# Performance work log

Measured on AMD Instinct MI355X. Metric: run time of the kernel, lower is better.

The kernel has to match this reference:

```python
import jax, jax.numpy as jnp
import numpy as np

B, L, D = 256, 256, 128          # batch, max_len, embedding_dim
H = W = 16                       # H=int(sqrt(L)), W=L//H
N, CBD = 128, 1024               # embedding_num, code_book_dim = N*8 = D*8
BETA = 0.25
BN_EPS = 1e-3                    # tf.layers.batch_normalization default


def _conv(x, w, b):
    return jax.lax.conv_general_dilated(x, w, (1, 1), 'VALID',
        dimension_numbers=('NHWC', 'HWIO', 'NHWC')) + b


def _convT(x, w, b):
    return jax.lax.conv_transpose(x, w, (1, 1), 'VALID',
        dimension_numbers=('NHWC', 'HWIO', 'NHWC')) + b


def _bn(x, g, b):
    # inference-mode BN with moving_mean=0, moving_var=1 (tf.layers default training=False)
    return g * (x * (1.0 / np.sqrt(1.0 + BN_EPS))) + b


def setup_inputs() -> dict:
    key = jax.random.key(0)
    ks = jax.random.split(key, 24)
    rn = lambda k, s, sc=0.05: (jax.random.normal(k, s, dtype=jnp.float32) * sc)
    inp = {
        'x': jax.random.normal(ks[0], (B, L, D), dtype=jnp.float32),
        'mask': jnp.ones((B, L), dtype=jnp.float32),
        'code_book': jax.random.normal(ks[1], (N, CBD), dtype=jnp.float32),
        # encoder: conv2d k=2 valid, channels D -> 2D -> 4D -> 8D
        'ew1': rn(ks[2], (2, 2, D, 2 * D)), 'eb1': jnp.zeros((2 * D,), jnp.float32),
        'eg1': jnp.ones((2 * D,), jnp.float32), 'ebt1': jnp.zeros((2 * D,), jnp.float32),
        'ew2': rn(ks[3], (2, 2, 2 * D, 4 * D)), 'eb2': jnp.zeros((4 * D,), jnp.float32),
        'eg2': jnp.ones((4 * D,), jnp.float32), 'ebt2': jnp.zeros((4 * D,), jnp.float32),
        'ew3': rn(ks[4], (2, 2, 4 * D, 8 * D)), 'eb3': jnp.zeros((8 * D,), jnp.float32),
        # decoder: conv2d_transpose k=2 valid, channels 8D -> 4D -> 2D -> D
        'dw1': rn(ks[5], (2, 2, 8 * D, 4 * D)), 'db1': jnp.zeros((4 * D,), jnp.float32),
        'dg1': jnp.ones((4 * D,), jnp.float32), 'dbt1': jnp.zeros((4 * D,), jnp.float32),
        'dw2': rn(ks[6], (2, 2, 4 * D, 2 * D)), 'db2': jnp.zeros((2 * D,), jnp.float32),
        'dg2': jnp.ones((2 * D,), jnp.float32), 'dbt2': jnp.zeros((2 * D,), jnp.float32),
        'dw3': rn(ks[7], (2, 2, 2 * D, D)), 'db3': jnp.zeros((D,), jnp.float32),
    }
    return inp


def reference(x, mask, code_book,
              ew1, eb1, eg1, ebt1, ew2, eb2, eg2, ebt2, ew3, eb3,
              dw1, db1, dg1, dbt1, dw2, db2, dg2, dbt2, dw3, db3):
    # ---- encoder (conv branch) ----
    xi = x.reshape(-1, H, W, D)                                   # [B,16,16,D]
    h = jax.nn.relu(_bn(_conv(xi, ew1, eb1), eg1, ebt1))          # [B,15,15,2D]
    h = jax.nn.relu(_bn(_conv(h, ew2, eb2), eg2, ebt2))           # [B,14,14,4D]
    x_encode = _conv(h, ew3, eb3)                                 # [B,13,13,8D]

    # ---- VQ codebook lookup (get_quantized) ----
    flat = x_encode.reshape(-1, CBD)                              # [B*169, CBD]
    dist = (jnp.sum(flat ** 2, axis=1, keepdims=True)
            + jnp.sum(code_book ** 2, axis=1)
            - 2.0 * flat @ code_book.T)                           # [B*169, N]
    idx = jnp.argmin(dist, axis=1)
    quantized = code_book[idx].reshape(x_encode.shape)            # gather == one_hot @ code_book

    # ---- straight-through + decoder ----
    ste = x_encode + jax.lax.stop_gradient(quantized - x_encode)
    h = jax.nn.relu(_bn(_convT(ste, dw1, db1), dg1, dbt1))        # [B,14,14,4D]
    h = jax.nn.relu(_bn(_convT(h, dw2, db2), dg2, dbt2))          # [B,15,15,2D]
    vq = _convT(h, dw3, db3)                                      # [B,16,16,D]
    vq_x = vq.reshape(-1, L, D)

    vq_mean = jnp.sum(vq_x, axis=1) / jnp.sum(mask, axis=-1, keepdims=True)

    recon = jnp.mean((x - vq_x) ** 2)
    vq_l = jnp.mean((quantized - jax.lax.stop_gradient(x_encode)) ** 2)
    commit = jnp.mean((x_encode - jax.lax.stop_gradient(quantized)) ** 2)
    vqvae_loss = recon + vq_l + BETA * commit
    return (vq_mean, vq_x, x_encode, quantized, vqvae_loss)
```

## Files before the change

### kernel.cpp

```cpp
#include <hip/hip_runtime.h>
#include <math.h>

typedef float f4 __attribute__((ext_vector_type(4)));
typedef short s8 __attribute__((ext_vector_type(8)));

#define WS_FLOATS 66000000L
__device__ float g_fallback[WS_FLOATS];

__device__ __forceinline__ f4 ldg4(const float* p) { return *(const f4*)p; }

__device__ __forceinline__ unsigned short bfr(float x) {
    unsigned int u = __float_as_uint(x);
    u += 0x7fffu + ((u >> 16) & 1u);
    return (unsigned short)(u >> 16);
}
__device__ __forceinline__ float bff(unsigned short h) {
    return __uint_as_float(((unsigned int)h) << 16);
}
__device__ __forceinline__ s8 z8() { s8 z = {0,0,0,0,0,0,0,0}; return z; }

__device__ __forceinline__ void split8(const f4& x0, const f4& x1, s8& hi, s8& lo) {
#pragma unroll
    for (int e = 0; e < 4; ++e) {
        unsigned short h0 = bfr(x0[e]);
        hi[e] = (short)h0; lo[e] = (short)bfr(x0[e] - bff(h0));
        unsigned short h1 = bfr(x1[e]);
        hi[e + 4] = (short)h1; lo[e + 4] = (short)bfr(x1[e] - bff(h1));
    }
}

template<int SPLIT, int ASRC, int EPI, int OUTF>
__global__ __launch_bounds__(256, 2)
void mfma_conv(const void* __restrict__ aHi, const void* __restrict__ aLo,
               const short* __restrict__ wHi, const short* __restrict__ wLo,
               const float* __restrict__ bias, const float* __restrict__ gamma,
               const float* __restrict__ beta,
               void* __restrict__ oHi, void* __restrict__ oLo,
               int* __restrict__ idxo,
               int IH, int IW, int Cin, int cinShift, int OHOW, int OW,
               int N, int K, int off, float bns)
{
    constexpr int PL = 128 * 64;
    __shared__ short smem[2 * SPLIT * PL];
    short* Ah = smem;
    short* Al = smem + PL;
    short* Bh = smem + SPLIT * PL;
    short* Bl = smem + SPLIT * PL + PL;

    const int tid = threadIdx.x;
    const int lane = tid & 63, wid = tid >> 6;
    const int fr = lane & 15, fq = lane >> 4;
    const int wm = (wid >> 1) * 64, wn = (wid & 1) * 64;
    const int m0 = blockIdx.x * 128, n0 = blockIdx.y * 128;

    const int sr = tid >> 1;
    const int skh = (tid & 1) << 5;

    long tapOff[4]; bool tv[4];
    {
        int m = m0 + sr;
        int b = m / OHOW; int rem = m - b * OHOW;
        int oi = rem / OW; int oj = rem - oi * OW;
#pragma unroll
        for (int t = 0; t < 4; ++t) {
            int ii = oi + (t >> 1) + off, jj = oj + (t & 1) + off;
            bool v = (ii >= 0) && (ii < IH) && (jj >= 0) && (jj < IW);
            tv[t] = v;
            tapOff[t] = ((long)b * IH + (v ? ii : 0)) * IW + (v ? jj : 0);
        }
    }

    f4 acc[4][4];
#pragma unroll
    for (int a = 0; a < 4; ++a)
#pragma unroll
        for (int b = 0; b < 4; ++b) acc[a][b] = (f4){0.f, 0.f, 0.f, 0.f};

    const short* wHrow = wHi + (long)(n0 + sr) * K;
    const short* wLrow = (SPLIT == 2) ? (wLo + (long)(n0 + sr) * K) : nullptr;

    const int swzW = (sr & 7) << 3;
    const int sbase = sr * 64;

    s8 rah[4], ral[4], rbh[4], rbl[4];
    f4 rax0[4], rax1[4];

    auto LOADREGS = [&](int kc) {
        const int kk = kc + skh;
        const int t = kk >> cinShift;
        const int ci = kk & (Cin - 1);
        const bool v = tv[t];
        if (ASRC == 0) {
            const float* p = (const float*)aHi + tapOff[t] * Cin + ci;
#pragma unroll
            for (int q = 0; q < 4; ++q) {
                rax0[q] = v ? ldg4(p + 8 * q) : (f4){0.f,0.f,0.f,0.f};
                rax1[q] = v ? ldg4(p + 8 * q + 4) : (f4){0.f,0.f,0.f,0.f};
            }
        } else if (ASRC == 1) {
            const short* ph = (const short*)aHi + tapOff[t] * Cin + ci;
            const short* pl = (const short*)aLo + tapOff[t] * Cin + ci;
#pragma unroll
            for (int q = 0; q < 4; ++q) {
                rah[q] = v ? *(const s8*)(ph + 8 * q) : z8();
                ral[q] = v ? *(const s8*)(pl + 8 * q) : z8();
            }
        } else {
            const short* ph = (const short*)aHi + tapOff[t] * Cin + ci;
#pragma unroll
            for (int q = 0; q < 4; ++q) rah[q] = v ? *(const s8*)(ph + 8 * q) : z8();
        }
#pragma unroll
        for (int q = 0; q < 4; ++q) {
            rbh[q] = *(const s8*)(wHrow + kc + skh + 8 * q);
            if (SPLIT == 2) rbl[q] = *(const s8*)(wLrow + kc + skh + 8 * q);
        }
    };

    auto STORE = [&]() {
        if (ASRC == 0) {
#pragma unroll
            for (int q = 0; q < 4; ++q) split8(rax0[q], rax1[q], rah[q], ral[q]);
        }
#pragma unroll
        for (int q = 0; q < 4; ++q) {
            int kx = (skh + 8 * q) ^ swzW;
            *(s8*)&Ah[sbase + kx] = rah[q];
            if (SPLIT == 2) *(s8*)&Al[sbase + kx] = ral[q];
            *(s8*)&Bh[sbase + kx] = rbh[q];
            if (SPLIT == 2) *(s8*)&Bl[sbase + kx] = rbl[q];
        }
    };

    LOADREGS(0);
    for (int kc = 0; kc < K; kc += 64) {
        __syncthreads();
        STORE();
        __syncthreads();
        if (kc + 64 < K) LOADREGS(kc + 64);

        __builtin_amdgcn_s_setprio(1);
#pragma unroll
        for (int ks = 0; ks < 2; ++ks) {
            const int colk = ks * 32 + fq * 8;
            s8 afh[4], afl[4], bfh[4], bfl[4];
#pragma unroll
            for (int mf = 0; mf < 4; ++mf) {
                int ar = wm + mf * 16 + fr;
                int ai = ar * 64 + (colk ^ ((ar & 7) << 3));
                afh[mf] = *(const s8*)&Ah[ai];
                if (SPLIT == 2) afl[mf] = *(const s8*)&Al[ai];
            }
#pragma unroll
            for (int nf = 0; nf < 4; ++nf) {
                int br = wn + nf * 16 + fr;
                int bi2 = br * 64 + (colk ^ ((br & 7) << 3));
                bfh[nf] = *(const s8*)&Bh[bi2];
                if (SPLIT == 2) bfl[nf] = *(const s8*)&Bl[bi2];
            }
#pragma unroll
            for (int mf = 0; mf < 4; ++mf)
#pragma unroll
                for (int nf = 0; nf < 4; ++nf) {
                    acc[mf][nf] = __builtin_amdgcn_mfma_f32_16x16x32_bf16(
                        afh[mf], bfh[nf], acc[mf][nf], 0, 0, 0);
                    if (SPLIT == 2) {
                        acc[mf][nf] = __builtin_amdgcn_mfma_f32_16x16x32_bf16(
                            afh[mf], bfl[nf], acc[mf][nf], 0, 0, 0);
                        acc[mf][nf] = __builtin_amdgcn_mfma_f32_16x16x32_bf16(
                            afl[mf], bfh[nf], acc[mf][nf], 0, 0, 0);
                    }
                }
        }
        __builtin_amdgcn_s_setprio(0);
    }

    if (EPI == 2) {
        __syncthreads();
        float* pbv = (float*)smem;
        int*   piv = (int*)((float*)smem + 256);
        float cnv[4];
#pragma unroll
        for (int nf = 0; nf < 4; ++nf) cnv[nf] = bias[n0 + wn + nf * 16 + fr];
#pragma unroll
        for (int mf = 0; mf < 4; ++mf)
#pragma unroll
            for (int j = 0; j < 4; ++j) {
                float best = 3.4e38f; int bi = 0;
#pragma unroll
                for (int nf = 0; nf < 4; ++nf) {
                    float d = cnv[nf] - 2.0f * acc[mf][nf][j];
                    int col = wn + nf * 16 + fr;
                    if (d < best) { best = d; bi = col; }
                }
#pragma unroll
                for (int sh = 1; sh <= 8; sh <<= 1) {
                    float ov = __shfl_xor(best, sh, 64);
                    int ob = __shfl_xor(bi, sh, 64);
                    if (ov < best || (ov == best && ob < bi)) { best = ov; bi = ob; }
                }
                if (fr == 0) {
                    int r = wm + mf * 16 + fq * 4 + j;
                    pbv[(wid & 1) * 128 + r] = best;
                    piv[(wid & 1) * 128 + r] = bi;
                }
            }
        __syncthreads();
        if (tid < 128) {
            float b0 = pbv[tid], b1 = pbv[128 + tid];
            int i0 = piv[tid], i1 = piv[128 + tid];
            idxo[m0 + tid] = (b1 < b0) ? i1 : i0;
        }
        return;
    }

    float bi[4], ga[4], be[4];
#pragma unroll
    for (int nf = 0; nf < 4; ++nf) {
        int col = n0 + wn + nf * 16 + fr;
        bi[nf] = bias[col];
        if (EPI == 1) { ga[nf] = gamma[col]; be[nf] = beta[col]; }
    }
#pragma unroll
    for (int mf = 0; mf < 4; ++mf)
#pragma unroll
        for (int j = 0; j < 4; ++j) {
            long gm = m0 + wm + mf * 16 + fq * 4 + j;
#pragma unroll
            for (int nf = 0; nf < 4; ++nf) {
                int col = n0 + wn + nf * 16 + fr;
                float vv = acc[mf][nf][j] + bi[nf];
                if (EPI == 1) {
                    vv = ga[nf] * (vv * bns) + be[nf];
                    vv = fmaxf(vv, 0.f);
                }
                long o = gm * (long)N + col;
                if (OUTF == 0) {
                    ((float*)oHi)[o] = vv;
                } else if (OUTF == 2) {
                    ((short*)oHi)[o] = (short)bfr(vv);
                } else {
                    unsigned short h = bfr(vv);
                    ((short*)oHi)[o] = (short)h;
                    ((short*)oLo)[o] = (short)bfr(vv - bff(h));
                }
            }
        }
}

__global__ void wprep(const float* __restrict__ w, short* __restrict__ hi,
                      short* __restrict__ lo, int kshift, int total, int N)
{
    int i = blockIdx.x * 256 + threadIdx.x;
    if (i >= total) return;
    int K = 1 << kshift;
    int n = i >> kshift, k = i & (K - 1);
    float x = w[(long)k * N + n];
    unsigned short h = bfr(x);
    hi[i] = (short)h;
    if (lo) lo[i] = (short)bfr(x - bff(h));
}

__global__ void dw1Tprep(const float* __restrict__ w, short* __restrict__ hi,
                         short* __restrict__ lo)
{
    int i = blockIdx.x * 256 + threadIdx.x;
    if (i >= 2097152) return;
    int Np = i >> 10, co = i & 1023;
    int t = Np >> 9, nn = Np & 511;
    float x = w[((long)(t * 1024 + co)) * 512 + nn];
    unsigned short h = bfr(x);
    hi[i] = (short)h;
    lo[i] = (short)bfr(x - bff(h));
}

__global__ void cbprep(const float* __restrict__ cb, short* __restrict__ hi,
                       short* __restrict__ lo)
{
    int i = blockIdx.x * 256 + threadIdx.x;
    float x = cb[i];
    unsigned short h = bfr(x);
    hi[i] = (short)h;
    lo[i] = (short)bfr(x - bff(h));
}

__global__ void wsplitT(const float* __restrict__ p1, short* __restrict__ hi,
                        short* __restrict__ lo)
{
    int i = blockIdx.x * 256 + threadIdx.x;
    if (i >= 262144) return;
    int n = i >> 11, k = i & 2047;
    float x = p1[(long)k * 128 + n];
    unsigned short h = bfr(x);
    hi[i] = (short)h;
    lo[i] = (short)bfr(x - bff(h));
}

__global__ void code_bias(const float* __restrict__ cb, const float* __restrict__ eb3,
                          float* __restrict__ bias2)
{
    int c = blockIdx.x * 4 + (threadIdx.x >> 6);
    int lane = threadIdx.x & 63;
    if (c >= 128) return;
    const f4* p = (const f4*)(cb + (long)c * 1024);
    const f4* e = (const f4*)eb3;
    float s2 = 0.f, su = 0.f;
#pragma unroll
    for (int q = 0; q < 4; ++q) {
        f4 v = p[q * 64 + lane];
        f4 w = e[q * 64 + lane];
        s2 += (v[0]*v[0] + v[1]*v[1]) + (v[2]*v[2] + v[3]*v[3]);
        su += (v[0]*w[0] + v[1]*w[1]) + (v[2]*w[2] + v[3]*w[3]);
    }
#pragma unroll
    for (int sh = 32; sh; sh >>= 1) {
        s2 += __shfl_xor(s2, sh, 64);
        su += __shfl_xor(su, sh, 64);
    }
    if (lane == 0) bias2[c] = s2 - 2.f * su;
}

__global__ __launch_bounds__(256)
void d1_gather(const float* __restrict__ CD, const int* __restrict__ idx,
               const float* __restrict__ db1, const float* __restrict__ dg1,
               const float* __restrict__ dbt1, short* __restrict__ out, float bns)
{
    int m = blockIdx.x * 4 + (threadIdx.x >> 6);
    int lane = threadIdx.x & 63;
    if (m >= 50176) return;
    int b = m / 196, rem = m - b * 196;
    int oi = rem / 14, oj = rem - oi * 14;
    float2 acc[4];
#pragma unroll
    for (int q = 0; q < 4; ++q) acc[q] = make_float2(0.f, 0.f);
#pragma unroll
    for (int t = 0; t < 4; ++t) {
        int ii = oi - 1 + (t >> 1), jj = oj - 1 + (t & 1);
        if (ii >= 0 && ii < 13 && jj >= 0 && jj < 13) {
            int c = idx[(b * 13 + ii) * 13 + jj];
            const float2* p = (const float2*)(CD + ((long)c * 2048 + t * 512));
#pragma unroll
            for (int q = 0; q < 4; ++q) {
                float2 v = p[lane + 64 * q];
                acc[q].x += v.x; acc[q].y += v.y;
            }
        }
    }
#pragma unroll
    for (int q = 0; q < 4; ++q) {
        int n = 2 * (lane + 64 * q);
        float v0 = fmaxf(dg1[n]     * ((acc[q].x + db1[n])     * bns) + dbt1[n],     0.f);
        float v1 = fmaxf(dg1[n + 1] * ((acc[q].y + db1[n + 1]) * bns) + dbt1[n + 1], 0.f);
        short2 s2v;
        s2v.x = (short)bfr(v0); s2v.y = (short)bfr(v1);
        ((short2*)out)[(long)m * 256 + lane + 64 * q] = s2v;
    }
}

__global__ __launch_bounds__(256)
void gather_sq(const float* __restrict__ cb, const int* __restrict__ idx,
               const float* __restrict__ xe, float* __restrict__ q,
               double* __restrict__ part, int rows)
{
    __shared__ double red[256];
    double s = 0.0;
    for (int m = blockIdx.x; m < rows; m += gridDim.x) {
        int c = idx[m];
        const f4* src = (const f4*)(cb + (long)c * 1024);
        const f4* xs  = (const f4*)(xe + (long)m * 1024);
        f4* dst = (f4*)(q + (long)m * 1024);
        f4 v = src[threadIdx.x];
        f4 xv = xs[threadIdx.x];
        dst[threadIdx.x] = v;
        f4 d = v - xv;
        s += ((double)d[0]*d[0] + (double)d[1]*d[1]) + ((double)d[2]*d[2] + (double)d[3]*d[3]);
    }
    red[threadIdx.x] = s; __syncthreads();
    for (int h = 128; h; h >>= 1) {
        if (threadIdx.x < h) red[threadIdx.x] += red[threadIdx.x + h];
        __syncthreads();
    }
    if (threadIdx.x == 0) part[blockIdx.x] = red[0];
}

__global__ void sqdiff_partial(const float* __restrict__ a, const float* __restrict__ b,
                               double* __restrict__ part, long n4)
{
    __shared__ double red[256];
    long i = (long)blockIdx.x * blockDim.x + threadIdx.x;
    long stride = (long)gridDim.x * blockDim.x;
    const f4* A = (const f4*)a;
    const f4* B = (const f4*)b;
    f4 s = (f4){0.f, 0.f, 0.f, 0.f};
    for (; i < n4; i += stride) {
        f4 d = A[i] - B[i];
        s += d * d;
    }
    double t = ((double)s[0] + s[1]) + ((double)s[2] + s[3]);
    red[threadIdx.x] = t;
    __syncthreads();
    for (int h = 128; h; h >>= 1) {
        if (threadIdx.x < h) red[threadIdx.x] += red[threadIdx.x + h];
        __syncthreads();
    }
    if (threadIdx.x == 0) part[blockIdx.x] = red[0];
}

__global__ void finalize_k(const double* __restrict__ pa, int na,
                           const double* __restrict__ pb, int nb,
                           float* __restrict__ loss)
{
    __shared__ double red[256];
    int t = threadIdx.x;
    double sa = 0;
    for (int i = t; i < na; i += 256) sa += pa[i];
    red[t] = sa; __syncthreads();
    for (int h = 128; h; h >>= 1) { if (t < h) red[t] += red[t + h]; __syncthreads(); }
    double SA = red[0];
    __syncthreads();
    double sb = 0;
    for (int i = t; i < nb; i += 256) sb += pb[i];
    red[t] = sb; __syncthreads();
    for (int h = 128; h; h >>= 1) { if (t < h) red[t] += red[t + h]; __syncthreads(); }
    if (t == 0) {
        double recon = SA / 8388608.0;
        double vql = red[0] / 44302336.0;
        loss[0] = (float)(recon + 1.25 * vql);
    }
}

__global__ void vq_mean_k(const float* __restrict__ vqx, const float* __restrict__ mask,
                          float* __restrict__ o)
{
    __shared__ float red[128];
    int b = blockIdx.x;
    int d = threadIdx.x;
    red[d] = mask[b * 256 + d] + mask[b * 256 + 128 + d];
    __syncthreads();
    for (int h = 64; h; h >>= 1) { if (d < h) red[d] += red[d + h]; __syncthreads(); }
    float msum = red[0];
    const float* p = vqx + (long)b * 256 * 128 + d;
    float s = 0.f;
    for (int l = 0; l < 256; ++l) s += p[l * 128];
    o[b * 128 + d] = s / msum;
}

extern "C" void kernel_launch(void* const* d_in, const int* in_sizes, int n_in,
                              void* d_out, int out_size, void* d_ws, size_t ws_size,
                              hipStream_t stream)
{
    const float* x    = (const float*)d_in[0];
    const float* mask = (const float*)d_in[1];
    const float* cb   = (const float*)d_in[2];
    const float* ew1 = (const float*)d_in[3];
    const float* eb1 = (const float*)d_in[4];
    const float* eg1 = (const float*)d_in[5];
    const float* ebt1= (const float*)d_in[6];
    const float* ew2 = (const float*)d_in[7];
    const float* eb2 = (const float*)d_in[8];
    const float* eg2 = (const float*)d_in[9];
    const float* ebt2= (const float*)d_in[10];
    const float* ew3 = (const float*)d_in[11];
    const float* eb3 = (const float*)d_in[12];
    const float* dw1 = (const float*)d_in[13];
    const float* db1 = (const float*)d_in[14];
    const float* dg1 = (const float*)d_in[15];
    const float* dbt1= (const float*)d_in[16];
    const float* dw2 = (const float*)d_in[17];
    const float* db2 = (const float*)d_in[18];
    const float* dg2 = (const float*)d_in[19];
    const float* dbt2= (const float*)d_in[20];
    const float* dw3 = (const float*)d_in[21];
    const float* db3 = (const float*)d_in[22];

    float* out = (float*)d_out;
    float* o_vqmean = out;
    float* o_vqx    = out + 32768;
    float* o_xe     = out + 8421376;
    float* o_q      = out + 52723712;
    float* o_loss   = out + 97026048;

    float* base;
    if (ws_size >= (size_t)WS_FLOATS * 4) {
        base = (float*)d_ws;
    } else {
        void* p = nullptr;
        hipGetSymbolAddress(&p, HIP_SYMBOL(g_fallback));
        base = (float*)p;
    }

    float* cur = base;
    short* h1h = (short*)cur; cur += 7372800;
    short* h1l = (short*)cur; cur += 7372800;
    short* h2h = (short*)cur; cur += 12845056;
    short* h2l = (short*)cur; cur += 12845056;
    short* d1o = (short*)cur; cur += 12845056;
    short* d2o = (short*)cur; cur += 7372800;
    short* ewt1h = (short*)cur; cur += 65536;
    short* ewt1l = (short*)cur; cur += 65536;
    short* ewt2h = (short*)cur; cur += 262144;
    short* ewt2l = (short*)cur; cur += 262144;
    short* ewt3h = (short*)cur; cur += 1048576;
    short* dwt1Th = (short*)cur; cur += 1048576;
    short* dwt1Tl = (short*)cur; cur += 1048576;
    short* dwt2h = (short*)cur; cur += 262144;
    short* dwt3h = (short*)cur; cur += 65536;
    short* cbh   = (short*)cur; cur += 65536;
    short* cbl   = (short*)cur; cur += 65536;
    float* P1raw = cur; cur += 262144;
    short* wvh   = (short*)cur; cur += 131072;
    short* wvl   = (short*)cur; cur += 131072;
    float* CDt   = cur; cur += 262144;
    float* bias2 = cur; cur += 128;
    float* zbuf  = cur; cur += 2048;
    int* idxb = (int*)cur; cur += 43264;
    double* pa = (double*)cur; cur += 4096;
    double* pq = (double*)cur; cur += 4096;

    const float bns = (float)(1.0 / sqrt(1.0 + 1e-3));

    hipMemsetAsync(zbuf, 0, 2048 * sizeof(float), stream);
    wprep<<<512, 256, 0, stream>>>(ew1, ewt1h, ewt1l, 9, 131072, 256);
    wprep<<<2048, 256, 0, stream>>>(ew2, ewt2h, ewt2l, 10, 524288, 512);
    wprep<<<8192, 256, 0, stream>>>(ew3, ewt3h, nullptr, 11, 2097152, 1024);
    dw1Tprep<<<8192, 256, 0, stream>>>(dw1, dwt1Th, dwt1Tl);
    wprep<<<2048, 256, 0, stream>>>(dw2, dwt2h, nullptr, 11, 524288, 256);
    wprep<<<512, 256, 0, stream>>>(dw3, dwt3h, nullptr, 10, 131072, 128);
    cbprep<<<512, 256, 0, stream>>>(cb, cbh, cbl);
    code_bias<<<32, 256, 0, stream>>>(cb, eb3, bias2);

    mfma_conv<2, 0, 0, 0><<<dim3(16, 1), 256, 0, stream>>>(
        ew3, nullptr, cbh, cbl, zbuf, nullptr, nullptr, P1raw, nullptr, nullptr,
        2, 2050, 1024, 10, 2048, 2048, 128, 1024, 0, bns);
    wsplitT<<<1024, 256, 0, stream>>>(P1raw, wvh, wvl);
    mfma_conv<2, 0, 0, 0><<<dim3(1, 16), 256, 0, stream>>>(
        cb, nullptr, dwt1Th, dwt1Tl, zbuf, nullptr, nullptr, CDt, nullptr, nullptr,
        2, 130, 1024, 10, 128, 128, 2048, 1024, 0, bns);

    mfma_conv<2, 0, 1, 1><<<dim3(450, 2), 256, 0, stream>>>(
        x, nullptr, ewt1h, ewt1l, eb1, eg1, ebt1, h1h, h1l, nullptr,
        16, 16, 128, 7, 225, 15, 256, 512, 0, bns);
    mfma_conv<2, 1, 1, 1><<<dim3(392, 4), 256, 0, stream>>>(
        h1h, h1l, ewt2h, ewt2l, eb2, eg2, ebt2, h2h, h2l, nullptr,
        15, 15, 256, 8, 196, 14, 512, 1024, 0, bns);
    mfma_conv<1, 2, 0, 0><<<dim3(338, 8), 256, 0, stream>>>(
        h2h, nullptr, ewt3h, nullptr, eb3, nullptr, nullptr, o_xe, nullptr, nullptr,
        14, 14, 512, 9, 169, 13, 1024, 2048, 0, bns);

    mfma_conv<2, 1, 2, 0><<<dim3(338, 1), 256, 0, stream>>>(
        h2h, h2l, wvh, wvl, bias2, nullptr, nullptr, nullptr, nullptr, idxb,
        14, 14, 512, 9, 169, 13, 128, 2048, 0, bns);
    gather_sq<<<2048, 256, 0, stream>>>(cb, idxb, o_xe, o_q, pq, 43264);

    d1_gather<<<12544, 256, 0, stream>>>(CDt, idxb, db1, dg1, dbt1, d1o, bns);
    mfma_conv<1, 2, 1, 2><<<dim3(450, 2), 256, 0, stream>>>(
        d1o, nullptr, dwt2h, nullptr, db2, dg2, dbt2, d2o, nullptr, nullptr,
        14, 14, 512, 9, 225, 15, 256, 2048, -1, bns);
    mfma_conv<1, 2, 0, 0><<<dim3(512, 1), 256, 0, stream>>>(
        d2o, nullptr, dwt3h, nullptr, db3, nullptr, nullptr, o_vqx, nullptr, nullptr,
        15, 15, 256, 8, 256, 16, 128, 1024, -1, bns);

    vq_mean_k<<<256, 128, 0, stream>>>(o_vqx, mask, o_vqmean);
    sqdiff_partial<<<1024, 256, 0, stream>>>(x, o_vqx, pa, 2097152L);
    finalize_k<<<1, 256, 0, stream>>>(pa, 1024, pq, 2048, o_loss);
}
```

Baseline: 1.045 ms.

## Merge weight-prep kernels, swap grid axes for N-fastest order, raise occupancy hint

```diff
diff --git a/kernel.cpp b/kernel.cpp
--- a/kernel.cpp
+++ b/kernel.cpp
@@ -30,7 +30,7 @@
 }
 
 template<int SPLIT, int ASRC, int EPI, int OUTF>
-__global__ __launch_bounds__(256, 2)
+__global__ __launch_bounds__(256, (SPLIT == 1 ? 4 : 2))
 void mfma_conv(const void* __restrict__ aHi, const void* __restrict__ aLo,
                const short* __restrict__ wHi, const short* __restrict__ wLo,
                const float* __restrict__ bias, const float* __restrict__ gamma,
@@ -51,7 +51,7 @@
     const int lane = tid & 63, wid = tid >> 6;
     const int fr = lane & 15, fq = lane >> 4;
     const int wm = (wid >> 1) * 64, wn = (wid & 1) * 64;
-    const int m0 = blockIdx.x * 128, n0 = blockIdx.y * 128;
+    const int m0 = blockIdx.y * 128, n0 = blockIdx.x * 128;
 
     const int sr = tid >> 1;
     const int skh = (tid & 1) << 5;
@@ -248,40 +248,49 @@
         }
 }
 
-__global__ void wprep(const float* __restrict__ w, short* __restrict__ hi,
-                      short* __restrict__ lo, int kshift, int total, int N)
-{
-    int i = blockIdx.x * 256 + threadIdx.x;
-    if (i >= total) return;
-    int K = 1 << kshift;
-    int n = i >> kshift, k = i & (K - 1);
-    float x = w[(long)k * N + n];
-    unsigned short h = bfr(x);
-    hi[i] = (short)h;
-    if (lo) lo[i] = (short)bfr(x - bff(h));
-}
-
-__global__ void dw1Tprep(const float* __restrict__ w, short* __restrict__ hi,
-                         short* __restrict__ lo)
-{
-    int i = blockIdx.x * 256 + threadIdx.x;
-    if (i >= 2097152) return;
-    int Np = i >> 10, co = i & 1023;
-    int t = Np >> 9, nn = Np & 511;
-    float x = w[((long)(t * 1024 + co)) * 512 + nn];
-    unsigned short h = bfr(x);
-    hi[i] = (short)h;
-    lo[i] = (short)bfr(x - bff(h));
-}
-
-__global__ void cbprep(const float* __restrict__ cb, short* __restrict__ hi,
-                       short* __restrict__ lo)
-{
-    int i = blockIdx.x * 256 + threadIdx.x;
-    float x = cb[i];
-    unsigned short h = bfr(x);
-    hi[i] = (short)h;
-    lo[i] = (short)bfr(x - bff(h));
+__global__ void prep_all(const float* __restrict__ ew1, const float* __restrict__ ew2,
+                         const float* __restrict__ ew3, const float* __restrict__ dw1,
+                         const float* __restrict__ dw2, const float* __restrict__ dw3,
+                         const float* __restrict__ cb,
+                         short* __restrict__ ewt1h, short* __restrict__ ewt1l,
+                         short* __restrict__ ewt2h, short* __restrict__ ewt2l,
+                         short* __restrict__ ewt3h,
+                         short* __restrict__ dwt1Th, short* __restrict__ dwt1Tl,
+                         short* __restrict__ dwt2h, short* __restrict__ dwt3h,
+                         short* __restrict__ cbh, short* __restrict__ cbl,
+                         float* __restrict__ zbuf)
+{
+    int b = blockIdx.x;
+    int t = threadIdx.x;
+    if (b < 512) {
+        int i = b * 256 + t; int n = i >> 9, k = i & 511;
+        float x = ew1[(long)k * 256 + n]; unsigned short h = bfr(x);
+        ewt1h[i] = (short)h; ewt1l[i] = (short)bfr(x - bff(h));
+    } else if (b < 2560) {
+        int i = (b - 512) * 256 + t; int n = i >> 10, k = i & 1023;
+        float x = ew2[(long)k * 512 + n]; unsigned short h = bfr(x);
+        ewt2h[i] = (short)h; ewt2l[i] = (short)bfr(x - bff(h));
+    } else if (b < 10752) {
+        int i = (b - 2560) * 256 + t; int n = i >> 11, k = i & 2047;
+        ewt3h[i] = (short)bfr(ew3[(long)k * 1024 + n]);
+    } else if (b < 18944) {
+        int i = (b - 10752) * 256 + t; int Np = i >> 10, co = i & 1023;
+        int tt = Np >> 9, nn = Np & 511;
+        float x = dw1[((long)(tt * 1024 + co)) * 512 + nn]; unsigned short h = bfr(x);
+        dwt1Th[i] = (short)h; dwt1Tl[i] = (short)bfr(x - bff(h));
+    } else if (b < 20992) {
+        int i = (b - 18944) * 256 + t; int n = i >> 11, k = i & 2047;
+        dwt2h[i] = (short)bfr(dw2[(long)k * 256 + n]);
+    } else if (b < 21504) {
+        int i = (b - 20992) * 256 + t; int n = i >> 10, k = i & 1023;
+        dwt3h[i] = (short)bfr(dw3[(long)k * 128 + n]);
+    } else if (b < 22016) {
+        int i = (b - 21504) * 256 + t;
+        float x = cb[i]; unsigned short h = bfr(x);
+        cbh[i] = (short)h; cbl[i] = (short)bfr(x - bff(h));
+    } else {
+        int i = (b - 22016) * 256 + t; if (i < 2048) zbuf[i] = 0.f;
+    }
 }
 
 __global__ void wsplitT(const float* __restrict__ p1, short* __restrict__ hi,
@@ -519,44 +528,39 @@
 
     const float bns = (float)(1.0 / sqrt(1.0 + 1e-3));
 
-    hipMemsetAsync(zbuf, 0, 2048 * sizeof(float), stream);
-    wprep<<<512, 256, 0, stream>>>(ew1, ewt1h, ewt1l, 9, 131072, 256);
-    wprep<<<2048, 256, 0, stream>>>(ew2, ewt2h, ewt2l, 10, 524288, 512);
-    wprep<<<8192, 256, 0, stream>>>(ew3, ewt3h, nullptr, 11, 2097152, 1024);
-    dw1Tprep<<<8192, 256, 0, stream>>>(dw1, dwt1Th, dwt1Tl);
-    wprep<<<2048, 256, 0, stream>>>(dw2, dwt2h, nullptr, 11, 524288, 256);
-    wprep<<<512, 256, 0, stream>>>(dw3, dwt3h, nullptr, 10, 131072, 128);
-    cbprep<<<512, 256, 0, stream>>>(cb, cbh, cbl);
+    prep_all<<<22024, 256, 0, stream>>>(ew1, ew2, ew3, dw1, dw2, dw3, cb,
+        ewt1h, ewt1l, ewt2h, ewt2l, ewt3h, dwt1Th, dwt1Tl, dwt2h, dwt3h,
+        cbh, cbl, zbuf);
     code_bias<<<32, 256, 0, stream>>>(cb, eb3, bias2);
 
-    mfma_conv<2, 0, 0, 0><<<dim3(16, 1), 256, 0, stream>>>(
+    mfma_conv<2, 0, 0, 0><<<dim3(1, 16), 256, 0, stream>>>(
         ew3, nullptr, cbh, cbl, zbuf, nullptr, nullptr, P1raw, nullptr, nullptr,
         2, 2050, 1024, 10, 2048, 2048, 128, 1024, 0, bns);
     wsplitT<<<1024, 256, 0, stream>>>(P1raw, wvh, wvl);
-    mfma_conv<2, 0, 0, 0><<<dim3(1, 16), 256, 0, stream>>>(
+    mfma_conv<2, 0, 0, 0><<<dim3(16, 1), 256, 0, stream>>>(
         cb, nullptr, dwt1Th, dwt1Tl, zbuf, nullptr, nullptr, CDt, nullptr, nullptr,
         2, 130, 1024, 10, 128, 128, 2048, 1024, 0, bns);
 
-    mfma_conv<2, 0, 1, 1><<<dim3(450, 2), 256, 0, stream>>>(
+    mfma_conv<2, 0, 1, 1><<<dim3(2, 450), 256, 0, stream>>>(
         x, nullptr, ewt1h, ewt1l, eb1, eg1, ebt1, h1h, h1l, nullptr,
         16, 16, 128, 7, 225, 15, 256, 512, 0, bns);
-    mfma_conv<2, 1, 1, 1><<<dim3(392, 4), 256, 0, stream>>>(
+    mfma_conv<2, 1, 1, 1><<<dim3(4, 392), 256, 0, stream>>>(
         h1h, h1l, ewt2h, ewt2l, eb2, eg2, ebt2, h2h, h2l, nullptr,
         15, 15, 256, 8, 196, 14, 512, 1024, 0, bns);
-    mfma_conv<1, 2, 0, 0><<<dim3(338, 8), 256, 0, stream>>>(
+    mfma_conv<1, 2, 0, 0><<<dim3(8, 338), 256, 0, stream>>>(
         h2h, nullptr, ewt3h, nullptr, eb3, nullptr, nullptr, o_xe, nullptr, nullptr,
         14, 14, 512, 9, 169, 13, 1024, 2048, 0, bns);
 
-    mfma_conv<2, 1, 2, 0><<<dim3(338, 1), 256, 0, stream>>>(
+    mfma_conv<2, 1, 2, 0><<<dim3(1, 338), 256, 0, stream>>>(
         h2h, h2l, wvh, wvl, bias2, nullptr, nullptr, nullptr, nullptr, idxb,
         14, 14, 512, 9, 169, 13, 128, 2048, 0, bns);
     gather_sq<<<2048, 256, 0, stream>>>(cb, idxb, o_xe, o_q, pq, 43264);
 
     d1_gather<<<12544, 256, 0, stream>>>(CDt, idxb, db1, dg1, dbt1, d1o, bns);
-    mfma_conv<1, 2, 1, 2><<<dim3(450, 2), 256, 0, stream>>>(
+    mfma_conv<1, 2, 1, 2><<<dim3(2, 450), 256, 0, stream>>>(
         d1o, nullptr, dwt2h, nullptr, db2, dg2, dbt2, d2o, nullptr, nullptr,
         14, 14, 512, 9, 225, 15, 256, 2048, -1, bns);
-    mfma_conv<1, 2, 0, 0><<<dim3(512, 1), 256, 0, stream>>>(
+    mfma_conv<1, 2, 0, 0><<<dim3(1, 512), 256, 0, stream>>>(
         d2o, nullptr, dwt3h, nullptr, db3, nullptr, nullptr, o_vqx, nullptr, nullptr,
         15, 15, 256, 8, 256, 16, 128, 1024, -1, bns);
 
```

Measured after the change: 1.254 ms. +20.0%, slower.
